# Optimization experiments

Hardware: AMD Instinct MI355X
Metric: run time of the kernel (lower is better)

## Reference

```python
import jax, jax.numpy as jnp
import numpy as np

RADIUS = (0.1, 0.1, 0.1)  # radius_x, radius_y, radius_z (cube half-widths)
NSAMPLE = 32


def setup_inputs() -> dict:
    key = jax.random.key(0)
    k1, k2, k3 = jax.random.split(key, 3)
    B, Nb, Mb, C = 4, 16384, 4096, 64
    xyz = jax.random.uniform(k1, (B * Nb, 3), dtype=jnp.float32)
    new_xyz = jax.random.uniform(k2, (B * Mb, 3), dtype=jnp.float32)
    features = jax.random.normal(k3, (B * Nb, C), dtype=jnp.float32)
    xyz_batch_cnt = jnp.full((B,), Nb, dtype=jnp.int32)
    new_xyz_batch_cnt = jnp.full((B,), Mb, dtype=jnp.int32)
    return {
        "xyz": xyz,
        "xyz_batch_cnt": xyz_batch_cnt,
        "new_xyz": new_xyz,
        "new_xyz_batch_cnt": new_xyz_batch_cnt,
        "features": features,
    }


def _cube_query(xyz_b, new_b, rx, ry, rz, nsample):
    # xyz_b: (B, Nb, 3); new_b: (B, Mb, 3)
    Nb = xyz_b.shape[1]

    def per_batch(args):
        pts, qs = args  # (Nb,3), (Mb,3)
        # cube membership test per axis (avoid stacking a (Mb,Nb,3) tensor)
        mask = (
            (jnp.abs(qs[:, None, 0] - pts[None, :, 0]) < rx)
            & (jnp.abs(qs[:, None, 1] - pts[None, :, 1]) < ry)
            & (jnp.abs(qs[:, None, 2] - pts[None, :, 2]) < rz)
        )  # (Mb, Nb)
        # CUDA kernel keeps the FIRST nsample neighbors in point order:
        # score favors in-cube points, tie-broken by smallest index.
        score = jnp.where(mask, -jnp.arange(Nb, dtype=jnp.float32), -jnp.inf)
        vals, idx_local = jax.lax.top_k(score, nsample)  # (Mb, nsample)
        valid = jnp.isfinite(vals)  # non_padding
        return idx_local, valid

    # process one batch at a time to bound the MbxNb intermediate
    idx_l, valid = jax.lax.map(per_batch, (xyz_b, new_b))
    return idx_l, valid


def reference(xyz, xyz_batch_cnt, new_xyz, new_xyz_batch_cnt, features):
    rx, ry, rz = RADIUS
    nsample = NSAMPLE
    B = xyz_batch_cnt.shape[0]
    N, M = xyz.shape[0], new_xyz.shape[0]
    Nb, Mb = N // B, M // B  # equal counts per batch (matches setup_inputs)

    xyz_b = xyz.reshape(B, Nb, 3)
    new_b = new_xyz.reshape(B, Mb, 3)

    idx_l, valid = _cube_query(xyz_b, new_b, rx, ry, rz, nsample)
    # local -> global flattened indices (batch offsets)
    offsets = (jnp.arange(B, dtype=idx_l.dtype) * Nb)[:, None, None]
    idx = (idx_l + offsets).reshape(M, nsample)
    valid = valid.reshape(M, nsample)
    # torch zeroes idx for empty/padding slots before gather
    idx = jnp.where(valid, idx, 0)

    non_padding = valid.astype(features.dtype)  # (M, nsample)
    grouped = features[idx]  # (M, nsample, C) gather
    # empty_ball_mask + padding_mask zeroing, fused into one multiply
    grouped = grouped * non_padding[..., None]
    grouped = jnp.transpose(grouped, (0, 2, 1))  # (M, C, nsample)
    num_non_padding = jnp.sum(non_padding, axis=-1)  # (M,)
    return grouped, num_non_padding
```

## Files before the change

### kernel.cpp

```cpp
#include <hip/hip_runtime.h>

#define NSAMPLE 32
#define RADI 0.1f
#define WPB 4
#define NCELL 4
#define NBLKA 3
#define NBLK3 27
#define NSEG 16
#define CAP 3072

__device__ __forceinline__ int cell_of(float x) {
    int c = (int)(x * (float)NCELL);
    c = c < 0 ? 0 : c;
    return c > (NCELL - 1) ? (NCELL - 1) : c;
}

__global__ __launch_bounds__(256) void pack_xyz_kernel(
    const float* __restrict__ xyz, float4* __restrict__ xyz4, int N)
{
    const int i = blockIdx.x * blockDim.x + threadIdx.x;
    if (i < N) {
        float4 v;
        v.x = xyz[i * 3 + 0];
        v.y = xyz[i * 3 + 1];
        v.z = xyz[i * 3 + 2];
        v.w = 0.0f;
        xyz4[i] = v;
    }
}

__global__ __launch_bounds__(64 * WPB) void count_kernel(
    const float4* __restrict__ xyz4, const int* __restrict__ xyz_cnt,
    int* __restrict__ segcnt, int B)
{
    const int wave = threadIdx.x >> 6, lane = threadIdx.x & 63;
    const int gw = blockIdx.x * WPB + wave;
    if (gw >= B * NBLK3 * NSEG) return;
    const int seg = gw % NSEG;
    const int blk = (gw / NSEG) % NBLK3;
    const int b   = gw / (NSEG * NBLK3);
    const int bx = blk % 3, by = (blk / 3) % 3, bz = blk / 9;

    int xstart = 0;
    for (int i = 0; i < b; ++i) xstart += xyz_cnt[i];
    const int nb = xyz_cnt[b];
    const int seglen = (nb + NSEG - 1) / NSEG;
    const int p0 = seg * seglen;
    const int p1 = min(p0 + seglen, nb);

    int cnt = 0;
    for (int base = p0; base < p1; base += 256) {
        #pragma unroll
        for (int k = 0; k < 4; ++k) {
            const int p = base + k * 64 + lane;
            bool hit = false;
            if (p < p1) {
                const float4 v = xyz4[xstart + p];
                hit = ((unsigned)(cell_of(v.x) - bx) <= 1u) &
                      ((unsigned)(cell_of(v.y) - by) <= 1u) &
                      ((unsigned)(cell_of(v.z) - bz) <= 1u);
            }
            cnt += (int)__popcll(__ballot(hit));
        }
    }
    if (lane == 0) segcnt[gw] = cnt;
}

__global__ __launch_bounds__(64 * WPB) void fill_kernel(
    const float4* __restrict__ xyz4, const int* __restrict__ xyz_cnt,
    const int* __restrict__ segcnt, float4* __restrict__ blk_pts, int B)
{
    const int wave = threadIdx.x >> 6, lane = threadIdx.x & 63;
    const int gw = blockIdx.x * WPB + wave;
    if (gw >= B * NBLK3 * NSEG) return;
    const int seg = gw % NSEG;
    const int blk = (gw / NSEG) % NBLK3;
    const int b   = gw / (NSEG * NBLK3);
    const int bx = blk % 3, by = (blk / 3) % 3, bz = blk / 9;

    int xstart = 0;
    for (int i = 0; i < b; ++i) xstart += xyz_cnt[i];
    const int nb = xyz_cnt[b];
    const int seglen = (nb + NSEG - 1) / NSEG;
    const int p0 = seg * seglen;
    const int p1 = min(p0 + seglen, nb);

    int off = 0;
    const int sbase = (b * NBLK3 + blk) * NSEG;
    for (int s = 0; s < seg; ++s) off += segcnt[sbase + s];

    float4* __restrict__ dst = blk_pts + (size_t)(b * NBLK3 + blk) * CAP;
    const unsigned long long lt = (1ull << lane) - 1ull;

    int cnt = 0;
    for (int base = p0; base < p1; base += 256) {
        #pragma unroll
        for (int k = 0; k < 4; ++k) {
            const int p = base + k * 64 + lane;
            bool hit = false;
            float4 v;
            if (p < p1) {
                v = xyz4[xstart + p];
                hit = ((unsigned)(cell_of(v.x) - bx) <= 1u) &
                      ((unsigned)(cell_of(v.y) - by) <= 1u) &
                      ((unsigned)(cell_of(v.z) - bz) <= 1u);
            }
            const unsigned long long m = __ballot(hit);
            if (hit) {
                const int slot = off + cnt + (int)__popcll(m & lt);
                if (slot < CAP) {
                    v.w = __int_as_float(xstart + p);
                    dst[slot] = v;
                }
            }
            cnt += (int)__popcll(m);
        }
    }
}

__global__ __launch_bounds__(64 * WPB, 8) void query_kernel(
    const float4* __restrict__ blk_pts,
    const int*    __restrict__ segcnt,
    const float*  __restrict__ new_xyz,
    const int*    __restrict__ new_cnt,
    const float*  __restrict__ features,
    float* __restrict__ out_grouped,
    float* __restrict__ out_cnt,
    int B, int M, int C)
{
    const int wave = threadIdx.x >> 6;
    const int lane = threadIdx.x & 63;
    const int q = blockIdx.x * WPB + wave;
    if (q >= M) return;

    __shared__ int s_idx_all[WPB][NSAMPLE];
    int* __restrict__ s_idx = s_idx_all[wave];
    if (lane < NSAMPLE) s_idx[lane] = 0;

    int b = 0, qacc = 0;
    for (int i = 0; i < B; ++i) {
        const int qc = new_cnt[i];
        if (q < qacc + qc) { b = i; break; }
        qacc += qc;
    }

    const float qx = new_xyz[q * 3 + 0];
    const float qy = new_xyz[q * 3 + 1];
    const float qz = new_xyz[q * 3 + 2];

    const int bxq = min(max((int)floorf((qx - 0.1000005f) * (float)NCELL), 0), NBLKA - 1);
    const int byq = min(max((int)floorf((qy - 0.1000005f) * (float)NCELL), 0), NBLKA - 1);
    const int bzq = min(max((int)floorf((qz - 0.1000005f) * (float)NCELL), 0), NBLKA - 1);
    const int blk = bxq + 3 * byq + 9 * bzq;

    const int sbase = (b * NBLK3 + blk) * NSEG;
    int lcnt = 0;
    #pragma unroll
    for (int s = 0; s < NSEG; ++s) lcnt += segcnt[sbase + s];
    if (lcnt > CAP) lcnt = CAP;

    const float4* __restrict__ lp = blk_pts + (size_t)(b * NBLK3 + blk) * CAP;
    const unsigned long long lt = (1ull << lane) - 1ull;

    int found = 0, base = 0;
    const int nfull = lcnt & ~255;

    auto test_group = [&](const float4& v, bool inb) {
        const float m3 = fmaxf(fmaxf(fabsf(qx - v.x), fabsf(qy - v.y)),
                               fabsf(qz - v.z));
        const bool c = inb & (m3 < RADI);
        const unsigned long long m = __ballot(c);
        if (c) {
            const int slot = found + (int)__popcll(m & lt);
            if (slot < NSAMPLE) s_idx[slot] = __float_as_int(v.w);
        }
        found += (int)__popcll(m);
    };

    if (nfull > 0) {
        float4 A[4], Bb[4];
        #pragma unroll
        for (int k = 0; k < 4; ++k) A[k] = lp[k * 64 + lane];

        while (true) {
            int nxt = base + 256;
            if (nxt < nfull) {
                #pragma unroll
                for (int k = 0; k < 4; ++k) Bb[k] = lp[nxt + k * 64 + lane];
            }
            #pragma unroll
            for (int k = 0; k < 4; ++k) test_group(A[k], true);
            base = nxt;
            if (found >= NSAMPLE || base >= nfull) break;

            nxt = base + 256;
            if (nxt < nfull) {
                #pragma unroll
                for (int k = 0; k < 4; ++k) A[k] = lp[nxt + k * 64 + lane];
            }
            #pragma unroll
            for (int k = 0; k < 4; ++k) test_group(Bb[k], true);
            base = nxt;
            if (found >= NSAMPLE || base >= nfull) break;
        }
    }
    while (found < NSAMPLE && base < lcnt) {
        #pragma unroll
        for (int k = 0; k < 4; ++k) {
            const int p = base + k * 64 + lane;
            const bool inb = (p < lcnt);
            const float4 v = lp[inb ? p : 0];
            test_group(v, inb);
        }
        base += 256;
    }
    if (found > NSAMPLE) found = NSAMPLE;

    asm volatile("s_waitcnt lgkmcnt(0)" ::: "memory");
    __builtin_amdgcn_sched_barrier(0);

    const int s0  = 4 * (lane & 7);
    const int chi = lane >> 3;
    const int r0 = s_idx[s0 + 0];
    const int r1 = s_idx[s0 + 1];
    const int r2 = s_idx[s0 + 2];
    const int r3 = s_idx[s0 + 3];
    const float k0 = (s0 + 0) < found ? 1.0f : 0.0f;
    const float k1 = (s0 + 1) < found ? 1.0f : 0.0f;
    const float k2 = (s0 + 2) < found ? 1.0f : 0.0f;
    const float k3 = (s0 + 3) < found ? 1.0f : 0.0f;

    const float* __restrict__ f0p = features + (size_t)r0 * C;
    const float* __restrict__ f1p = features + (size_t)r1 * C;
    const float* __restrict__ f2p = features + (size_t)r2 * C;
    const float* __restrict__ f3p = features + (size_t)r3 * C;

    float* __restrict__ og = out_grouped + (size_t)q * (C * NSAMPLE);
    #pragma unroll
    for (int k = 0; k < 8; ++k) {
        const int c = 8 * k + chi;
        float4 v;
        v.x = f0p[c] * k0;
        v.y = f1p[c] * k1;
        v.z = f2p[c] * k2;
        v.w = f3p[c] * k3;
        *reinterpret_cast<float4*>(og + (size_t)(k * 64 + lane) * 4) = v;
    }
    if (lane == 0) out_cnt[q] = (float)found;
}

__global__ __launch_bounds__(64 * WPB, 8) void fallback_kernel(
    const float* __restrict__ xyz, const int* __restrict__ xyz_cnt,
    const float* __restrict__ new_xyz, const int* __restrict__ new_cnt,
    const float* __restrict__ features,
    float* __restrict__ out_grouped, float* __restrict__ out_cnt,
    int B, int M, int C)
{
    const int wave = threadIdx.x >> 6, lane = threadIdx.x & 63;
    const int q = blockIdx.x * WPB + wave;
    if (q >= M) return;

    __shared__ int s_idx_all[WPB][NSAMPLE];
    int* __restrict__ s_idx = s_idx_all[wave];
    if (lane < NSAMPLE) s_idx[lane] = 0;

    int b = 0, qacc = 0, xstart = 0;
    for (int i = 0; i < B; ++i) {
        const int qc = new_cnt[i];
        if (q < qacc + qc) { b = i; break; }
        qacc += qc; xstart += xyz_cnt[i];
    }
    const int nb = xyz_cnt[b];
    const float qx = new_xyz[q * 3 + 0], qy = new_xyz[q * 3 + 1], qz = new_xyz[q * 3 + 2];
    const float* __restrict__ xp = xyz + (size_t)xstart * 3;
    const unsigned long long lt = (1ull << lane) - 1ull;

    int found = 0;
    for (int base = 0; base < nb && found < NSAMPLE; base += 64) {
        const int p = base + lane;
        bool c = false;
        if (p < nb) {
            const float dx = qx - xp[p * 3 + 0];
            const float dy = qy - xp[p * 3 + 1];
            const float dz = qz - xp[p * 3 + 2];
            c = (fabsf(dx) < RADI) && (fabsf(dy) < RADI) && (fabsf(dz) < RADI);
        }
        const unsigned long long m = __ballot(c);
        if (c) {
            const int slot = found + (int)__popcll(m & lt);
            if (slot < NSAMPLE) s_idx[slot] = xstart + p;
        }
        found += (int)__popcll(m);
    }
    if (found > NSAMPLE) found = NSAMPLE;

    asm volatile("s_waitcnt lgkmcnt(0)" ::: "memory");
    __builtin_amdgcn_sched_barrier(0);

    const int s0 = 4 * (lane & 7), chi = lane >> 3;
    const int r0 = s_idx[s0 + 0], r1 = s_idx[s0 + 1], r2 = s_idx[s0 + 2], r3 = s_idx[s0 + 3];
    const float k0 = (s0 + 0) < found ? 1.0f : 0.0f;
    const float k1 = (s0 + 1) < found ? 1.0f : 0.0f;
    const float k2 = (s0 + 2) < found ? 1.0f : 0.0f;
    const float k3 = (s0 + 3) < found ? 1.0f : 0.0f;
    const float* f0p = features + (size_t)r0 * C;
    const float* f1p = features + (size_t)r1 * C;
    const float* f2p = features + (size_t)r2 * C;
    const float* f3p = features + (size_t)r3 * C;
    float* __restrict__ og = out_grouped + (size_t)q * (C * NSAMPLE);
    #pragma unroll
    for (int k = 0; k < 8; ++k) {
        const int c = 8 * k + chi;
        float4 v;
        v.x = f0p[c] * k0; v.y = f1p[c] * k1; v.z = f2p[c] * k2; v.w = f3p[c] * k3;
        *reinterpret_cast<float4*>(og + (size_t)(k * 64 + lane) * 4) = v;
    }
    if (lane == 0) out_cnt[q] = (float)found;
}

extern "C" void kernel_launch(void* const* d_in, const int* in_sizes, int n_in,
                              void* d_out, int out_size, void* d_ws, size_t ws_size,
                              hipStream_t stream) {
    const float* xyz      = (const float*)d_in[0];
    const int*   xyz_cnt  = (const int*)d_in[1];
    const float* new_xyz  = (const float*)d_in[2];
    const int*   new_cnt  = (const int*)d_in[3];
    const float* features = (const float*)d_in[4];

    const int B = in_sizes[1];
    const int N = in_sizes[0] / 3;
    const int M = in_sizes[2] / 3;
    const int C = in_sizes[4] / N;

    float* out_grouped = (float*)d_out;
    float* out_cnt     = (float*)d_out + (size_t)M * C * NSAMPLE;

    const size_t pack_bytes = (size_t)N * sizeof(float4);
    const size_t blk_bytes  = (size_t)B * NBLK3 * CAP * sizeof(float4);
    const size_t seg_bytes  = (size_t)B * NBLK3 * NSEG * sizeof(int);
    const size_t need = pack_bytes + blk_bytes + seg_bytes;

    if (ws_size >= need) {
        float4* xyz4    = (float4*)d_ws;
        float4* blk_pts = (float4*)((char*)d_ws + pack_bytes);
        int*    segcnt  = (int*)((char*)d_ws + pack_bytes + blk_bytes);

        hipLaunchKernelGGL(pack_xyz_kernel, dim3((N + 255) / 256), dim3(256), 0, stream,
                           xyz, xyz4, N);
        const int nbw = B * NBLK3 * NSEG;
        hipLaunchKernelGGL(count_kernel, dim3((nbw + WPB - 1) / WPB), dim3(64 * WPB), 0, stream,
                           xyz4, xyz_cnt, segcnt, B);
        hipLaunchKernelGGL(fill_kernel, dim3((nbw + WPB - 1) / WPB), dim3(64 * WPB), 0, stream,
                           xyz4, xyz_cnt, segcnt, blk_pts, B);
        hipLaunchKernelGGL(query_kernel, dim3((M + WPB - 1) / WPB), dim3(64 * WPB), 0, stream,
                           blk_pts, segcnt, new_xyz, new_cnt, features,
                           out_grouped, out_cnt, B, M, C);
    } else {
        hipLaunchKernelGGL(fallback_kernel, dim3((M + WPB - 1) / WPB), dim3(64 * WPB), 0, stream,
                           xyz, xyz_cnt, new_xyz, new_cnt, features,
                           out_grouped, out_cnt, B, M, C);
    }
}
```

Baseline: 76.90 us.

## Raise segment count, precompute block counts, early-exit query, nontemporal output stores

```diff
diff --git a/kernel.cpp b/kernel.cpp
--- a/kernel.cpp
+++ b/kernel.cpp
@@ -3,11 +3,16 @@
 #define NSAMPLE 32
 #define RADI 0.1f
 #define WPB 4
+#define MARGIN 0.0002f
+
 #define NCELL 4
 #define NBLKA 3
+#define SPAN  2
 #define NBLK3 27
-#define NSEG 16
-#define CAP 3072
+#define CAP   3072
+#define NSEG  64
+
+typedef float nat_f32x4 __attribute__((ext_vector_type(4)));
 
 __device__ __forceinline__ int cell_of(float x) {
     int c = (int)(x * (float)NCELL);
@@ -39,7 +44,7 @@
     const int seg = gw % NSEG;
     const int blk = (gw / NSEG) % NBLK3;
     const int b   = gw / (NSEG * NBLK3);
-    const int bx = blk % 3, by = (blk / 3) % 3, bz = blk / 9;
+    const int bx = blk % NBLKA, by = (blk / NBLKA) % NBLKA, bz = blk / (NBLKA * NBLKA);
 
     int xstart = 0;
     for (int i = 0; i < b; ++i) xstart += xyz_cnt[i];
@@ -56,9 +61,9 @@
             bool hit = false;
             if (p < p1) {
                 const float4 v = xyz4[xstart + p];
-                hit = ((unsigned)(cell_of(v.x) - bx) <= 1u) &
-                      ((unsigned)(cell_of(v.y) - by) <= 1u) &
-                      ((unsigned)(cell_of(v.z) - bz) <= 1u);
+                hit = ((unsigned)(cell_of(v.x) - bx) < (unsigned)SPAN) &
+                      ((unsigned)(cell_of(v.y) - by) < (unsigned)SPAN) &
+                      ((unsigned)(cell_of(v.z) - bz) < (unsigned)SPAN);
             }
             cnt += (int)__popcll(__ballot(hit));
         }
@@ -68,7 +73,8 @@
 
 __global__ __launch_bounds__(64 * WPB) void fill_kernel(
     const float4* __restrict__ xyz4, const int* __restrict__ xyz_cnt,
-    const int* __restrict__ segcnt, float4* __restrict__ blk_pts, int B)
+    const int* __restrict__ segcnt, float4* __restrict__ blk_pts,
+    int* __restrict__ blkcnt, int B)
 {
     const int wave = threadIdx.x >> 6, lane = threadIdx.x & 63;
     const int gw = blockIdx.x * WPB + wave;
@@ -76,7 +82,7 @@
     const int seg = gw % NSEG;
     const int blk = (gw / NSEG) % NBLK3;
     const int b   = gw / (NSEG * NBLK3);
-    const int bx = blk % 3, by = (blk / 3) % 3, bz = blk / 9;
+    const int bx = blk % NBLKA, by = (blk / NBLKA) % NBLKA, bz = blk / (NBLKA * NBLKA);
 
     int xstart = 0;
     for (int i = 0; i < b; ++i) xstart += xyz_cnt[i];
@@ -85,11 +91,12 @@
     const int p0 = seg * seglen;
     const int p1 = min(p0 + seglen, nb);
 
+    const int bid = b * NBLK3 + blk;
     int off = 0;
-    const int sbase = (b * NBLK3 + blk) * NSEG;
+    const int sbase = bid * NSEG;
     for (int s = 0; s < seg; ++s) off += segcnt[sbase + s];
 
-    float4* __restrict__ dst = blk_pts + (size_t)(b * NBLK3 + blk) * CAP;
+    float4* __restrict__ dst = blk_pts + (size_t)bid * CAP;
     const unsigned long long lt = (1ull << lane) - 1ull;
 
     int cnt = 0;
@@ -101,9 +108,9 @@
             float4 v;
             if (p < p1) {
                 v = xyz4[xstart + p];
-                hit = ((unsigned)(cell_of(v.x) - bx) <= 1u) &
-                      ((unsigned)(cell_of(v.y) - by) <= 1u) &
-                      ((unsigned)(cell_of(v.z) - bz) <= 1u);
+                hit = ((unsigned)(cell_of(v.x) - bx) < (unsigned)SPAN) &
+                      ((unsigned)(cell_of(v.y) - by) < (unsigned)SPAN) &
+                      ((unsigned)(cell_of(v.z) - bz) < (unsigned)SPAN);
             }
             const unsigned long long m = __ballot(hit);
             if (hit) {
@@ -116,11 +123,12 @@
             cnt += (int)__popcll(m);
         }
     }
+    if (seg == NSEG - 1 && lane == 0) blkcnt[bid] = off + cnt;
 }
 
 __global__ __launch_bounds__(64 * WPB, 8) void query_kernel(
     const float4* __restrict__ blk_pts,
-    const int*    __restrict__ segcnt,
+    const int*    __restrict__ blkcnt,
     const float*  __restrict__ new_xyz,
     const int*    __restrict__ new_cnt,
     const float*  __restrict__ features,
@@ -148,18 +156,15 @@
     const float qy = new_xyz[q * 3 + 1];
     const float qz = new_xyz[q * 3 + 2];
 
-    const int bxq = min(max((int)floorf((qx - 0.1000005f) * (float)NCELL), 0), NBLKA - 1);
-    const int byq = min(max((int)floorf((qy - 0.1000005f) * (float)NCELL), 0), NBLKA - 1);
-    const int bzq = min(max((int)floorf((qz - 0.1000005f) * (float)NCELL), 0), NBLKA - 1);
-    const int blk = bxq + 3 * byq + 9 * bzq;
-
-    const int sbase = (b * NBLK3 + blk) * NSEG;
-    int lcnt = 0;
-    #pragma unroll
-    for (int s = 0; s < NSEG; ++s) lcnt += segcnt[sbase + s];
+    const int bxq = min(max((int)floorf((qx - RADI - MARGIN) * (float)NCELL), 0), NBLKA - 1);
+    const int byq = min(max((int)floorf((qy - RADI - MARGIN) * (float)NCELL), 0), NBLKA - 1);
+    const int bzq = min(max((int)floorf((qz - RADI - MARGIN) * (float)NCELL), 0), NBLKA - 1);
+    const int bid = b * NBLK3 + bxq + NBLKA * byq + NBLKA * NBLKA * bzq;
+
+    int lcnt = blkcnt[bid];
     if (lcnt > CAP) lcnt = CAP;
 
-    const float4* __restrict__ lp = blk_pts + (size_t)(b * NBLK3 + blk) * CAP;
+    const float4* __restrict__ lp = blk_pts + (size_t)bid * CAP;
     const unsigned long long lt = (1ull << lane) - 1ull;
 
     int found = 0, base = 0;
@@ -189,7 +194,10 @@
                 for (int k = 0; k < 4; ++k) Bb[k] = lp[nxt + k * 64 + lane];
             }
             #pragma unroll
-            for (int k = 0; k < 4; ++k) test_group(A[k], true);
+            for (int k = 0; k < 4; ++k) {
+                test_group(A[k], true);
+                if (found >= NSAMPLE) break;
+            }
             base = nxt;
             if (found >= NSAMPLE || base >= nfull) break;
 
@@ -199,7 +207,10 @@
                 for (int k = 0; k < 4; ++k) A[k] = lp[nxt + k * 64 + lane];
             }
             #pragma unroll
-            for (int k = 0; k < 4; ++k) test_group(Bb[k], true);
+            for (int k = 0; k < 4; ++k) {
+                test_group(Bb[k], true);
+                if (found >= NSAMPLE) break;
+            }
             base = nxt;
             if (found >= NSAMPLE || base >= nfull) break;
         }
@@ -239,12 +250,13 @@
     #pragma unroll
     for (int k = 0; k < 8; ++k) {
         const int c = 8 * k + chi;
-        float4 v;
+        nat_f32x4 v;
         v.x = f0p[c] * k0;
         v.y = f1p[c] * k1;
         v.z = f2p[c] * k2;
         v.w = f3p[c] * k3;
-        *reinterpret_cast<float4*>(og + (size_t)(k * 64 + lane) * 4) = v;
+        __builtin_nontemporal_store(v,
+            reinterpret_cast<nat_f32x4*>(og + (size_t)(k * 64 + lane) * 4));
     }
     if (lane == 0) out_cnt[q] = (float)found;
 }
@@ -338,12 +350,14 @@
     const size_t pack_bytes = (size_t)N * sizeof(float4);
     const size_t blk_bytes  = (size_t)B * NBLK3 * CAP * sizeof(float4);
     const size_t seg_bytes  = (size_t)B * NBLK3 * NSEG * sizeof(int);
-    const size_t need = pack_bytes + blk_bytes + seg_bytes;
+    const size_t bcn_bytes  = (size_t)B * NBLK3 * sizeof(int);
+    const size_t need = pack_bytes + blk_bytes + seg_bytes + bcn_bytes;
 
     if (ws_size >= need) {
         float4* xyz4    = (float4*)d_ws;
         float4* blk_pts = (float4*)((char*)d_ws + pack_bytes);
         int*    segcnt  = (int*)((char*)d_ws + pack_bytes + blk_bytes);
+        int*    blkcnt  = (int*)((char*)d_ws + pack_bytes + blk_bytes + seg_bytes);
 
         hipLaunchKernelGGL(pack_xyz_kernel, dim3((N + 255) / 256), dim3(256), 0, stream,
                            xyz, xyz4, N);
@@ -351,9 +365,9 @@
         hipLaunchKernelGGL(count_kernel, dim3((nbw + WPB - 1) / WPB), dim3(64 * WPB), 0, stream,
                            xyz4, xyz_cnt, segcnt, B);
         hipLaunchKernelGGL(fill_kernel, dim3((nbw + WPB - 1) / WPB), dim3(64 * WPB), 0, stream,
-                           xyz4, xyz_cnt, segcnt, blk_pts, B);
+                           xyz4, xyz_cnt, segcnt, blk_pts, blkcnt, B);
         hipLaunchKernelGGL(query_kernel, dim3((M + WPB - 1) / WPB), dim3(64 * WPB), 0, stream,
-                           blk_pts, segcnt, new_xyz, new_cnt, features,
+                           blk_pts, blkcnt, new_xyz, new_cnt, features,
                            out_grouped, out_cnt, B, M, C);
     } else {
         hipLaunchKernelGGL(fallback_kernel, dim3((M + WPB - 1) / WPB), dim3(64 * WPB), 0, stream,
```

Measured after the change: 74.04 us. 3.7% less time.
